# Kernel tuning notes

Hardware: AMD Instinct MI355X
Metric: run time of the kernel (lower is better)

Reference implementation:

```python
import jax, jax.numpy as jnp
import numpy as np
import math

N_HEAD = 16

def _rope(x):
    # x: [B, H, T, D], D even; interleaved-pair rotation as in the torch code
    B, H, T, D = x.shape
    theta = 10000.0 ** (-2.0 * jnp.arange(D // 2, dtype=x.dtype) / D)  # [D/2]
    pos = jnp.arange(T, dtype=x.dtype)[:, None]                        # [T,1]
    ang = pos * theta[None, :]                                          # [T, D/2]
    sin, cos = jnp.sin(ang), jnp.cos(ang)
    x1, x2 = x[..., ::2], x[..., 1::2]
    x1r = x1 * cos - x2 * sin
    x2r = x1 * sin + x2 * cos
    # re-interleave
    out = jnp.stack([x1r, x2r], axis=-1).reshape(B, H, T, D)
    return out

def setup_inputs() -> dict:
    key = jax.random.key(0)
    ks = jax.random.split(key, 3)
    B, T, C = 4, 2048, 1024
    x = jax.random.normal(ks[0], (B, T, C), dtype=jnp.float32)
    W_qkv = jax.random.normal(ks[1], (C, 3 * C), dtype=jnp.float32) * (1.0 / math.sqrt(C))
    b_qkv = jnp.zeros((3 * C,), dtype=jnp.float32)
    W_proj = jax.random.normal(ks[2], (C, C), dtype=jnp.float32) * (1.0 / math.sqrt(C))
    b_proj = jnp.zeros((C,), dtype=jnp.float32)
    return {"x": x, "W_qkv": W_qkv, "b_qkv": b_qkv, "W_proj": W_proj, "b_proj": b_proj}

def reference(x, W_qkv, b_qkv, W_proj, b_proj):
    B, T, C = x.shape
    H = N_HEAD
    D = C // H
    qkv = x @ W_qkv + b_qkv                      # [B,T,3C]
    q, k, v = jnp.split(qkv, 3, axis=-1)
    def to_heads(t):
        return t.reshape(B, T, H, D).transpose(0, 2, 1, 3)  # [B,H,T,D]
    q, k, v = to_heads(q), to_heads(k), to_heads(v)
    q = _rope(q)
    k = _rope(k)
    att = jnp.einsum('bhqd,bhkd->bhqk', q, k) * (1.0 / math.sqrt(D))
    mask = jnp.tril(jnp.ones((T, T), dtype=bool))
    att = jnp.where(mask[None, None, :, :], att, -jnp.inf)
    att = jax.nn.softmax(att, axis=-1)
    y = jnp.einsum('bhqk,bhkd->bhqd', att, v)    # [B,H,T,D]
    y = y.transpose(0, 2, 1, 3).reshape(B, T, C)
    return y @ W_proj + b_proj
```

## Files before the change

kernel.cpp:

```cpp
#include <hip/hip_runtime.h>
#include <cstddef>

#define B_DIM 4
#define T_DIM 2048
#define C_DIM 1024
#define H_DIM 16
#define D_DIM 64
#define C3_DIM 3072

typedef __attribute__((ext_vector_type(8))) _Float16 f16x8;
typedef __attribute__((ext_vector_type(4))) _Float16 f16x4;
typedef __attribute__((ext_vector_type(4))) float f32x4;

typedef const __attribute__((address_space(1))) unsigned int* gptr_t;
typedef __attribute__((address_space(3))) unsigned int* lptr_t;

#define QSCALE 0.180336850073f
#define NTHETA 0.41524101186f

__global__ __launch_bounds__(256) void prep(
    const float* __restrict__ x, _Float16* __restrict__ xh,
    const float* __restrict__ Wq, _Float16* __restrict__ Wqt,
    const float* __restrict__ Wp, _Float16* __restrict__ Wpt)
{
    __shared__ float tile[64][65];
    const int z = blockIdx.x, tid = threadIdx.x;

    if (z < 8192) {
        size_t i = (size_t)z * 1024 + tid * 4;
        float4 v = *(const float4*)&x[i];
        f16x4 o = { (_Float16)v.x, (_Float16)v.y, (_Float16)v.z, (_Float16)v.w };
        *(f16x4*)&xh[i] = o;
        return;
    }

    const float* W;
    _Float16* Wt;
    int N, idx;
    if (z < 8960) { W = Wq; Wt = Wqt; N = C3_DIM; idx = z - 8192; }
    else          { W = Wp; Wt = Wpt; N = C_DIM;  idx = z - 8960; }
    const int K = C_DIM;
    const int nblk = N / 64;
    const int n0 = (idx % nblk) * 64, k0 = (idx / nblk) * 64;

    const int tx = tid & 15, ty = tid >> 4;
#pragma unroll
    for (int it = 0; it < 4; ++it) {
        int r = it * 16 + ty;
        *(float4*)&tile[r][tx * 4] =
            *(const float4*)&W[(size_t)(k0 + r) * N + n0 + tx * 4];
    }
    __syncthreads();
    int c = tid >> 2, t0 = (tid & 3) * 16;
    __align__(16) _Float16 tmp[16];
#pragma unroll
    for (int j = 0; j < 16; ++j) tmp[j] = (_Float16)tile[t0 + j][c];
    _Float16* o = Wt + (size_t)(n0 + c) * K + k0 + t0;
    *(f16x8*)o = *(f16x8*)&tmp[0];
    *(f16x8*)(o + 8) = *(f16x8*)&tmp[8];
}

#define ISSUE_SLICE(BUF, S, KT)                                               \
    do {                                                                      \
        const _Float16* agk = ag + (KT) * 64 + (S) * 32;                      \
        const _Float16* bgk = bg + (KT) * 64 + (S) * 32;                      \
        __builtin_amdgcn_global_load_lds((gptr_t)(const void*)(agk),          \
            (lptr_t)(void*)&Af[BUF][S][w * 2 + 0][0][0], 16, 0, 0);           \
        __builtin_amdgcn_global_load_lds((gptr_t)(const void*)(agk + 16 * K), \
            (lptr_t)(void*)&Af[BUF][S][w * 2 + 1][0][0], 16, 0, 0);           \
        __builtin_amdgcn_global_load_lds((gptr_t)(const void*)(bgk),          \
            (lptr_t)(void*)&Bf[BUF][S][w][0][0], 16, 0, 0);                   \
    } while (0)

#define COMPUTE_SLICE(BUF, S, SWAPPED)                                        \
    do {                                                                      \
        f16x8 av[4], bv[4];                                                   \
        _Pragma("unroll")                                                     \
        for (int i = 0; i < 4; ++i) {                                         \
            av[i] = *(const f16x8*)&Af[BUF][S][wm * 4 + i][lane][0];          \
            bv[i] = *(const f16x8*)&Bf[BUF][S][wn * 4 + i][lane][0];          \
        }                                                                     \
        __builtin_amdgcn_s_setprio(1);                                        \
        _Pragma("unroll")                                                     \
        for (int i = 0; i < 4; ++i)                                           \
            _Pragma("unroll")                                                 \
            for (int j = 0; j < 4; ++j)                                       \
                acc[i][j] = (SWAPPED)                                         \
                    ? __builtin_amdgcn_mfma_f32_16x16x32_f16(                 \
                          bv[j], av[i], acc[i][j], 0, 0, 0)                   \
                    : __builtin_amdgcn_mfma_f32_16x16x32_f16(                 \
                          av[i], bv[j], acc[i][j], 0, 0, 0);                  \
        __builtin_amdgcn_s_setprio(0);                                        \
    } while (0)

#define KLOOP(SWAPPED)                                                        \
    do {                                                                      \
        const int NT = K / 64;                                                \
        ISSUE_SLICE(0, 0, 0);                                                 \
        ISSUE_SLICE(0, 1, 0);                                                 \
        for (int t = 0; t < NT; ++t) {                                        \
            const int cb = t & 1;                                             \
            asm volatile("s_waitcnt vmcnt(0)" ::: "memory");                  \
            __builtin_amdgcn_s_barrier();                                     \
            if (t + 1 < NT) {                                                 \
                ISSUE_SLICE(cb ^ 1, 0, t + 1);                                \
                ISSUE_SLICE(cb ^ 1, 1, t + 1);                                \
            }                                                                 \
            COMPUTE_SLICE(cb, 0, SWAPPED);                                    \
            COMPUTE_SLICE(cb, 1, SWAPPED);                                    \
        }                                                                     \
    } while (0)

__global__ __launch_bounds__(512, 2) void gemm_qkv(
    const _Float16* __restrict__ A, const _Float16* __restrict__ Bt,
    const float* __restrict__ bias,
    _Float16* __restrict__ Qb, _Float16* __restrict__ Kb, _Float16* __restrict__ Vt)
{
    __shared__ __align__(16) _Float16 Af[2][2][16][64][8];
    __shared__ __align__(16) _Float16 Bf[2][2][8][64][8];
    const int tid = threadIdx.x;
    const int lane = tid & 63, w = tid >> 6;
    const int lm = lane & 15, lq = lane >> 4;
    const int wm = w >> 1, wn = w & 1;
    const int m0 = blockIdx.y * 256, n0 = blockIdx.x * 128;
    const int K = C_DIM;

    const _Float16* ag = A + (size_t)(m0 + w * 32 + lm) * K + lq * 8;
    const _Float16* bg = Bt + (size_t)(n0 + w * 16 + lm) * K + lq * 8;

    f32x4 acc[4][4];
#pragma unroll
    for (int i = 0; i < 4; ++i)
#pragma unroll
        for (int j = 0; j < 4; ++j) acc[i][j] = (f32x4){0.f, 0.f, 0.f, 0.f};

    const bool is_v = (n0 >= 2 * C_DIM);

    if (!is_v) {
        KLOOP(true);

        const bool is_q = (n0 < C_DIM);
        const float scale = is_q ? QSCALE : 1.0f;
        _Float16* dstbase = is_q ? Qb : Kb;
#pragma unroll
        for (int j = 0; j < 4; ++j) {
            int col = n0 + wn * 64 + j * 16 + lq * 4;
            int d0 = col & 63;
            int h = (col & (C_DIM - 1)) >> 6;
            float4 b4 = *(const float4*)&bias[col];
            float th0 = exp2f(-NTHETA * (float)(d0 >> 1));
            float th1 = exp2f(-NTHETA * (float)((d0 >> 1) + 1));
#pragma unroll
            for (int i = 0; i < 4; ++i) {
                int tg = m0 + wm * 64 + i * 16 + lm;
                int bb = tg >> 11, tl = tg & (T_DIM - 1);
                float v0 = acc[i][j][0] + b4.x;
                float v1 = acc[i][j][1] + b4.y;
                float v2 = acc[i][j][2] + b4.z;
                float v3 = acc[i][j][3] + b4.w;
                float s0, c0, s1, c1;
                __sincosf((float)tl * th0, &s0, &c0);
                __sincosf((float)tl * th1, &s1, &c1);
                f16x4 o = { (_Float16)((v0 * c0 - v1 * s0) * scale),
                            (_Float16)((v0 * s0 + v1 * c0) * scale),
                            (_Float16)((v2 * c1 - v3 * s1) * scale),
                            (_Float16)((v2 * s1 + v3 * c1) * scale) };
                *(f16x4*)&dstbase[((size_t)(bb * 16 + h) * T_DIM + tl) * 64 + d0] = o;
            }
        }
    } else {
        KLOOP(false);

#pragma unroll
        for (int i = 0; i < 4; ++i) {
            int t4 = m0 + wm * 64 + i * 16 + lq * 4;
            int bb = t4 >> 11, tl = t4 & (T_DIM - 1);
#pragma unroll
            for (int j = 0; j < 4; ++j) {
                int col = n0 + wn * 64 + j * 16 + lm;
                int dfull = col - 2 * C_DIM;
                int h = dfull >> 6, d = dfull & 63;
                float bc = bias[col];
                f16x4 o = { (_Float16)(acc[i][j][0] + bc),
                            (_Float16)(acc[i][j][1] + bc),
                            (_Float16)(acc[i][j][2] + bc),
                            (_Float16)(acc[i][j][3] + bc) };
                *(f16x4*)&Vt[((size_t)(bb * 16 + h) * 64 + d) * T_DIM + tl] = o;
            }
        }
    }
}

template <bool OUT_HALF>
__global__ __launch_bounds__(512, 2) void gemm_bt(
    const _Float16* __restrict__ A, const _Float16* __restrict__ Bt,
    const float* __restrict__ bias, void* __restrict__ Cout,
    int M, int N, int K)
{
    __shared__ __align__(16) _Float16 Af[2][2][16][64][8];
    __shared__ __align__(16) _Float16 Bf[2][2][8][64][8];
    const int tid = threadIdx.x;
    const int lane = tid & 63, w = tid >> 6;
    const int lm = lane & 15, lq = lane >> 4;
    const int wm = w >> 1, wn = w & 1;
    const int m0 = blockIdx.y * 256, n0 = blockIdx.x * 128;

    const _Float16* ag = A + (size_t)(m0 + w * 32 + lm) * K + lq * 8;
    const _Float16* bg = Bt + (size_t)(n0 + w * 16 + lm) * K + lq * 8;

    f32x4 acc[4][4];
#pragma unroll
    for (int i = 0; i < 4; ++i)
#pragma unroll
        for (int j = 0; j < 4; ++j) acc[i][j] = (f32x4){0.f, 0.f, 0.f, 0.f};

    KLOOP(true);

#pragma unroll
    for (int i = 0; i < 4; ++i) {
        size_t row = (size_t)(m0 + wm * 64 + i * 16 + lm);
#pragma unroll
        for (int j = 0; j < 4; ++j) {
            int col = n0 + wn * 64 + j * 16 + lq * 4;
            float4 b4 = *(const float4*)&bias[col];
            float v0 = acc[i][j][0] + b4.x;
            float v1 = acc[i][j][1] + b4.y;
            float v2 = acc[i][j][2] + b4.z;
            float v3 = acc[i][j][3] + b4.w;
            if (OUT_HALF) {
                f16x4 o = { (_Float16)v0, (_Float16)v1, (_Float16)v2, (_Float16)v3 };
                *(f16x4*)&((_Float16*)Cout)[row * N + col] = o;
            } else {
                float4 o = make_float4(v0, v1, v2, v3);
                *(float4*)&((float*)Cout)[row * N + col] = o;
            }
        }
    }
}

__global__ __launch_bounds__(256) void attn_mfma(
    const _Float16* __restrict__ Qb, const _Float16* __restrict__ Kb,
    const _Float16* __restrict__ Vt, _Float16* __restrict__ yb)
{
    __shared__ __align__(16) _Float16 Kf[8][64][8];
    __shared__ __align__(16) _Float16 Vf[8][64][8];
    __shared__ __align__(16) _Float16 Pb[4][16][88];

    const int tid = threadIdx.x;
    const int bh = blockIdx.x;
    const int qt = 31 - blockIdx.y;
    const int b = bh >> 4, h = bh & 15;
    const int lane = tid & 63, w = tid >> 6;
    const int m = lane & 15, qq = lane >> 4;

    const _Float16* qrow = Qb +
        ((size_t)bh * T_DIM + qt * 64 + w * 16 + m) * D_DIM + qq * 8;
    f16x8 qreg[2];
    qreg[0] = *(const f16x8*)qrow;
    qreg[1] = *(const f16x8*)(qrow + 32);

    float l_i = 0.f;
    f32x4 acc[4];
#pragma unroll
    for (int db = 0; db < 4; ++db) acc[db] = (f32x4){0.f, 0.f, 0.f, 0.f};

    const _Float16* kg0 = Kb + (size_t)bh * T_DIM * D_DIM +
                          (size_t)(w * 16 + m) * D_DIM + qq * 8;
    const _Float16* vg0 = Vt + (size_t)bh * D_DIM * T_DIM +
                          (size_t)(w * 16 + m) * T_DIM + qq * 8;

    f16x8 kr0 = *(const f16x8*)(kg0);
    f16x8 kr1 = *(const f16x8*)(kg0 + 32);
    f16x8 vr0 = *(const f16x8*)(vg0);
    f16x8 vr1 = *(const f16x8*)(vg0 + 32);

    for (int kt = 0; kt <= qt; ++kt) {
        __syncthreads();
        *(f16x8*)&Kf[w * 2 + 0][lane][0] = kr0;
        *(f16x8*)&Kf[w * 2 + 1][lane][0] = kr1;
        *(f16x8*)&Vf[w * 2 + 0][lane][0] = vr0;
        *(f16x8*)&Vf[w * 2 + 1][lane][0] = vr1;
        __syncthreads();

        int ktn = (kt < qt) ? kt + 1 : kt;
        kr0 = *(const f16x8*)(kg0 + (size_t)ktn * 64 * D_DIM);
        kr1 = *(const f16x8*)(kg0 + (size_t)ktn * 64 * D_DIM + 32);
        vr0 = *(const f16x8*)(vg0 + ktn * 64);
        vr1 = *(const f16x8*)(vg0 + ktn * 64 + 32);

        f32x4 sv[4];
#pragma unroll
        for (int nb = 0; nb < 4; ++nb) {
            f32x4 s = (f32x4){0.f, 0.f, 0.f, 0.f};
            s = __builtin_amdgcn_mfma_f32_16x16x32_f16(
                *(const f16x8*)&Kf[nb * 2 + 0][lane][0], qreg[0], s, 0, 0, 0);
            s = __builtin_amdgcn_mfma_f32_16x16x32_f16(
                *(const f16x8*)&Kf[nb * 2 + 1][lane][0], qreg[1], s, 0, 0, 0);
            sv[nb] = s;
        }

        if (kt == qt) {
            int qlocal = w * 16 + m;
#pragma unroll
            for (int nb = 0; nb < 4; ++nb) {
                int tb = nb * 16 + qq * 4;
#pragma unroll
                for (int r = 0; r < 4; ++r)
                    if (tb + r > qlocal) sv[nb][r] = -1e30f;
            }
        }

        float ll = 0.f;
#pragma unroll
        for (int nb = 0; nb < 4; ++nb) {
            float p0 = exp2f(sv[nb][0]);
            float p1 = exp2f(sv[nb][1]);
            float p2 = exp2f(sv[nb][2]);
            float p3 = exp2f(sv[nb][3]);
            sv[nb][0] = p0; sv[nb][1] = p1; sv[nb][2] = p2; sv[nb][3] = p3;
            ll += (p0 + p1) + (p2 + p3);
        }
        l_i += ll;

#pragma unroll
        for (int nb = 0; nb < 4; ++nb) {
            f16x4 pv = { (_Float16)sv[nb][0], (_Float16)sv[nb][1],
                         (_Float16)sv[nb][2], (_Float16)sv[nb][3] };
            *(f16x4*)&Pb[w][m][nb * 16 + qq * 4] = pv;
        }

        f16x8 pf0 = *(const f16x8*)&Pb[w][m][0 * 32 + qq * 8];
        f16x8 pf1 = *(const f16x8*)&Pb[w][m][1 * 32 + qq * 8];

#pragma unroll
        for (int db = 0; db < 4; ++db) {
            acc[db] = __builtin_amdgcn_mfma_f32_16x16x32_f16(
                *(const f16x8*)&Vf[db * 2 + 0][lane][0], pf0, acc[db], 0, 0, 0);
            acc[db] = __builtin_amdgcn_mfma_f32_16x16x32_f16(
                *(const f16x8*)&Vf[db * 2 + 1][lane][0], pf1, acc[db], 0, 0, 0);
        }
    }

    l_i += __shfl_xor(l_i, 16);
    l_i += __shfl_xor(l_i, 32);

    float inv = 1.0f / l_i;
    _Float16* yrow = yb + (size_t)(b * T_DIM + qt * 64 + w * 16 + m) * C_DIM +
                     h * D_DIM + qq * 4;
#pragma unroll
    for (int db = 0; db < 4; ++db) {
        f16x4 o = { (_Float16)(acc[db][0] * inv), (_Float16)(acc[db][1] * inv),
                    (_Float16)(acc[db][2] * inv), (_Float16)(acc[db][3] * inv) };
        *(f16x4*)(yrow + db * 16) = o;
    }
}

extern "C" void kernel_launch(void* const* d_in, const int* in_sizes, int n_in,
                              void* d_out, int out_size, void* d_ws, size_t ws_size,
                              hipStream_t stream)
{
    const float* x     = (const float*)d_in[0];
    const float* Wqkv  = (const float*)d_in[1];
    const float* bqkv  = (const float*)d_in[2];
    const float* Wproj = (const float*)d_in[3];
    const float* bproj = (const float*)d_in[4];
    float* out = (float*)d_out;

    char* ws = (char*)d_ws;
    _Float16* xh  = (_Float16*)(ws);
    _Float16* yh  = (_Float16*)(ws + 16777216ull);
    _Float16* Qb  = (_Float16*)(ws + 33554432ull);
    _Float16* Kb  = (_Float16*)(ws + 50331648ull);
    _Float16* Vt  = (_Float16*)(ws + 67108864ull);
    _Float16* Wqt = (_Float16*)(ws + 83886080ull);
    _Float16* Wpt = (_Float16*)(ws + 90177536ull);

    prep<<<dim3(9216), dim3(256), 0, stream>>>(x, xh, Wqkv, Wqt, Wproj, Wpt);

    gemm_qkv<<<dim3(C3_DIM / 128, (B_DIM * T_DIM) / 256), dim3(512), 0, stream>>>(
        xh, Wqt, bqkv, Qb, Kb, Vt);

    attn_mfma<<<dim3(B_DIM * H_DIM, T_DIM / 64), dim3(256), 0, stream>>>(
        Qb, Kb, Vt, yh);

    gemm_bt<false><<<dim3(C_DIM / 128, (B_DIM * T_DIM) / 256), dim3(512), 0, stream>>>(
        yh, Wpt, bproj, out, B_DIM * T_DIM, C_DIM, C_DIM);
}
```

Before: 318.3 us.

## Deepen GEMM K-pipeline to a 6-slot LDS ring and swizzle blocks across XCDs

Both GEMM kernels replace the double-buffered 64-wide K tile with a 6-entry ring of 32-wide K slices. Loads are prefetched four slices ahead with graded vmcnt waits, so only one barrier per slice is needed and more global-load latency is hidden. Block indices are also remapped so consecutive blocks land on the same XCD, which is meant to improve L2 reuse of A and B tiles. The larger LDS footprint (about 144 KB per block) likely prevents two blocks from sharing a CU, which reduces occupancy.

```diff
diff --git a/kernel.cpp b/kernel.cpp
--- a/kernel.cpp
+++ b/kernel.cpp
@@ -60,25 +60,25 @@
     *(f16x8*)(o + 8) = *(f16x8*)&tmp[8];
 }
 
-#define ISSUE_SLICE(BUF, S, KT)                                               \
+#define ISSUE_SLICE(RB, S)                                                    \
     do {                                                                      \
-        const _Float16* agk = ag + (KT) * 64 + (S) * 32;                      \
-        const _Float16* bgk = bg + (KT) * 64 + (S) * 32;                      \
+        const _Float16* agk = ag + (S) * 32;                                  \
+        const _Float16* bgk = bg + (S) * 32;                                  \
         __builtin_amdgcn_global_load_lds((gptr_t)(const void*)(agk),          \
-            (lptr_t)(void*)&Af[BUF][S][w * 2 + 0][0][0], 16, 0, 0);           \
+            (lptr_t)(void*)&Af[RB][w * 2 + 0][0][0], 16, 0, 0);               \
         __builtin_amdgcn_global_load_lds((gptr_t)(const void*)(agk + 16 * K), \
-            (lptr_t)(void*)&Af[BUF][S][w * 2 + 1][0][0], 16, 0, 0);           \
+            (lptr_t)(void*)&Af[RB][w * 2 + 1][0][0], 16, 0, 0);               \
         __builtin_amdgcn_global_load_lds((gptr_t)(const void*)(bgk),          \
-            (lptr_t)(void*)&Bf[BUF][S][w][0][0], 16, 0, 0);                   \
+            (lptr_t)(void*)&Bf[RB][w][0][0], 16, 0, 0);                       \
     } while (0)
 
-#define COMPUTE_SLICE(BUF, S, SWAPPED)                                        \
+#define COMPUTE_SLICE(RB, SWAPPED)                                            \
     do {                                                                      \
         f16x8 av[4], bv[4];                                                   \
         _Pragma("unroll")                                                     \
         for (int i = 0; i < 4; ++i) {                                         \
-            av[i] = *(const f16x8*)&Af[BUF][S][wm * 4 + i][lane][0];          \
-            bv[i] = *(const f16x8*)&Bf[BUF][S][wn * 4 + i][lane][0];          \
+            av[i] = *(const f16x8*)&Af[RB][wm * 4 + i][lane][0];              \
+            bv[i] = *(const f16x8*)&Bf[RB][wn * 4 + i][lane][0];              \
         }                                                                     \
         __builtin_amdgcn_s_setprio(1);                                        \
         _Pragma("unroll")                                                     \
@@ -95,19 +95,29 @@
 
 #define KLOOP(SWAPPED)                                                        \
     do {                                                                      \
-        const int NT = K / 64;                                                \
-        ISSUE_SLICE(0, 0, 0);                                                 \
-        ISSUE_SLICE(0, 1, 0);                                                 \
-        for (int t = 0; t < NT; ++t) {                                        \
-            const int cb = t & 1;                                             \
-            asm volatile("s_waitcnt vmcnt(0)" ::: "memory");                  \
+        const int NS = K / 32;                                                \
+        ISSUE_SLICE(0, 0); ISSUE_SLICE(1, 1);                                 \
+        ISSUE_SLICE(2, 2); ISSUE_SLICE(3, 3);                                 \
+        int rb = 0, ri = 4;                                                   \
+        for (int s = 0; s < NS; ++s) {                                        \
+            if (s + 4 < NS) {                                                 \
+                ISSUE_SLICE(ri, s + 4);                                       \
+                asm volatile("s_waitcnt vmcnt(12)" ::: "memory");             \
+            } else {                                                          \
+                int rem = NS - 1 - s;                                         \
+                if (rem == 3)                                                 \
+                    asm volatile("s_waitcnt vmcnt(9)" ::: "memory");          \
+                else if (rem == 2)                                            \
+                    asm volatile("s_waitcnt vmcnt(6)" ::: "memory");          \
+                else if (rem == 1)                                            \
+                    asm volatile("s_waitcnt vmcnt(3)" ::: "memory");          \
+                else                                                          \
+                    asm volatile("s_waitcnt vmcnt(0)" ::: "memory");          \
+            }                                                                 \
             __builtin_amdgcn_s_barrier();                                     \
-            if (t + 1 < NT) {                                                 \
-                ISSUE_SLICE(cb ^ 1, 0, t + 1);                                \
-                ISSUE_SLICE(cb ^ 1, 1, t + 1);                                \
-            }                                                                 \
-            COMPUTE_SLICE(cb, 0, SWAPPED);                                    \
-            COMPUTE_SLICE(cb, 1, SWAPPED);                                    \
+            COMPUTE_SLICE(rb, SWAPPED);                                       \
+            ++rb; if (rb == 6) rb = 0;                                        \
+            ++ri; if (ri == 6) ri = 0;                                        \
         }                                                                     \
     } while (0)
 
@@ -116,14 +126,19 @@
     const float* __restrict__ bias,
     _Float16* __restrict__ Qb, _Float16* __restrict__ Kb, _Float16* __restrict__ Vt)
 {
-    __shared__ __align__(16) _Float16 Af[2][2][16][64][8];
-    __shared__ __align__(16) _Float16 Bf[2][2][8][64][8];
+    __shared__ __align__(16) _Float16 Af[6][16][64][8];
+    __shared__ __align__(16) _Float16 Bf[6][8][64][8];
     const int tid = threadIdx.x;
     const int lane = tid & 63, w = tid >> 6;
     const int lm = lane & 15, lq = lane >> 4;
     const int wm = w >> 1, wn = w & 1;
-    const int m0 = blockIdx.y * 256, n0 = blockIdx.x * 128;
     const int K = C_DIM;
+
+    const int nbx = gridDim.x;
+    const int lin = blockIdx.y * nbx + blockIdx.x;
+    const int cpx = (nbx * gridDim.y) >> 3;
+    const int swz = (lin & 7) * cpx + (lin >> 3);
+    const int m0 = (swz / nbx) * 256, n0 = (swz % nbx) * 128;
 
     const _Float16* ag = A + (size_t)(m0 + w * 32 + lm) * K + lq * 8;
     const _Float16* bg = Bt + (size_t)(n0 + w * 16 + lm) * K + lq * 8;
@@ -197,13 +212,18 @@
     const float* __restrict__ bias, void* __restrict__ Cout,
     int M, int N, int K)
 {
-    __shared__ __align__(16) _Float16 Af[2][2][16][64][8];
-    __shared__ __align__(16) _Float16 Bf[2][2][8][64][8];
+    __shared__ __align__(16) _Float16 Af[6][16][64][8];
+    __shared__ __align__(16) _Float16 Bf[6][8][64][8];
     const int tid = threadIdx.x;
     const int lane = tid & 63, w = tid >> 6;
     const int lm = lane & 15, lq = lane >> 4;
     const int wm = w >> 1, wn = w & 1;
-    const int m0 = blockIdx.y * 256, n0 = blockIdx.x * 128;
+
+    const int nbx = gridDim.x;
+    const int lin = blockIdx.y * nbx + blockIdx.x;
+    const int cpx = (nbx * gridDim.y) >> 3;
+    const int swz = (lin & 7) * cpx + (lin >> 3);
+    const int m0 = (swz / nbx) * 256, n0 = (swz % nbx) * 128;
 
     const _Float16* ag = A + (size_t)(m0 + w * 32 + lm) * K + lq * 8;
     const _Float16* bg = Bt + (size_t)(n0 + w * 16 + lm) * K + lq * 8;
```

New measurement: 290.3 us. 1.1x faster.
